# Optimization experiments

Hardware: AMD Instinct MI355X
Metric: run time of the kernel (lower is better)

Reference implementation:

```python
import jax, jax.numpy as jnp
import numpy as np

VOCAB, HIDDEN, LAYERS = 128, 1024, 2
B, T = 128, 512


def setup_inputs() -> dict:
    key = jax.random.key(0)
    ks = jax.random.split(key, 8)
    s0 = 1.0 / np.sqrt(HIDDEN)
    x = jax.random.normal(ks[0], (B, T, VOCAB), dtype=jnp.float32)
    h = jnp.zeros((LAYERS, B, HIDDEN), dtype=jnp.float32)
    c = jnp.zeros((LAYERS, B, HIDDEN), dtype=jnp.float32)
    # LSTM params, gate order (i, f, g, o) concatenated along last dim (4H)
    Wx0 = jax.random.uniform(ks[1], (VOCAB, 4 * HIDDEN), jnp.float32, -s0, s0)
    Wh0 = jax.random.uniform(ks[2], (HIDDEN, 4 * HIDDEN), jnp.float32, -s0, s0)
    b0 = jax.random.uniform(ks[3], (4 * HIDDEN,), jnp.float32, -s0, s0)
    Wx1 = jax.random.uniform(ks[4], (HIDDEN, 4 * HIDDEN), jnp.float32, -s0, s0)
    Wh1 = jax.random.uniform(ks[5], (HIDDEN, 4 * HIDDEN), jnp.float32, -s0, s0)
    b1 = jax.random.uniform(ks[6], (4 * HIDDEN,), jnp.float32, -s0, s0)
    return {"x": x, "h": h, "c": c, "Wx0": Wx0, "Wh0": Wh0, "b0": b0,
            "Wx1": Wx1, "Wh1": Wh1, "b1": b1}


def _lstm_cell(inp, h_prev, c_prev, Wx, Wh, b):
    gates = inp @ Wx + h_prev @ Wh + b            # (B, 4H)
    i, f, g, o = jnp.split(gates, 4, axis=-1)
    i = jax.nn.sigmoid(i)
    f = jax.nn.sigmoid(f)
    g = jnp.tanh(g)
    o = jax.nn.sigmoid(o)
    c_new = f * c_prev + i * g
    h_new = o * jnp.tanh(c_new)
    return h_new, c_new


def reference(x, h, c, Wx0, Wh0, b0, Wx1, Wh1, b1):
    layer_params = [(Wx0, Wh0, b0), (Wx1, Wh1, b1)]

    def step(carry, x_t):
        h_prev, c_prev = carry                    # each (L, B, H)
        inp = x_t                                 # (B, VOCAB)
        hs, cs = [], []
        for l, (Wx, Wh, b) in enumerate(layer_params):
            h_new, c_new = _lstm_cell(inp, h_prev[l], c_prev[l], Wx, Wh, b)
            hs.append(h_new)
            cs.append(c_new)
            inp = h_new
        return (jnp.stack(hs), jnp.stack(cs)), hs[-1]

    xs = jnp.swapaxes(x, 0, 1)                    # (T, B, VOCAB)
    (h_f, c_f), outs = jax.lax.scan(step, (h, c), xs)
    outs = jnp.swapaxes(outs, 0, 1)               # (B, T, H)
    return outs, h_f, c_f
```

## Files before the change

### kernel.cpp

```cpp
#include <hip/hip_runtime.h>

#define VV 128
#define HH 1024
#define BB 128
#define TT 512
#define G4 4096
#define BTH ((size_t)BB * TT * HH)
#define HPAR (4 * 64 * 512)
#define RING 32

typedef __attribute__((ext_vector_type(8))) short bf16x8;
typedef __attribute__((ext_vector_type(16))) float f32x16;

__device__ __forceinline__ short f2bf(float f) {
  unsigned u = __float_as_uint(f);
  u = (u + 0x7fffu + ((u >> 16) & 1u)) >> 16;
  return (short)u;
}

__device__ __forceinline__ float fsig(float x) {
  x = fminf(fmaxf(x, -30.f), 30.f);
  float e = __expf(-x);
  return 1.f / (1.f + e);
}
__device__ __forceinline__ float ftanh(float x) {
  x = fminf(fmaxf(x, -15.f), 15.f);
  float e = __expf(-2.f * x);
  return (1.f - e) / (1.f + e);
}

__device__ __forceinline__ unsigned eidx(int t) {
  return ((unsigned)(t + 1) * 37u) & (RING - 1);
}


__global__ void init_state(const float* __restrict__ h,
                           short* __restrict__ h0dst, short* __restrict__ h1dst) {
  const int n = 2 * HPAR;
  for (int i = blockIdx.x * blockDim.x + threadIdx.x; i < n; i += gridDim.x * blockDim.x) {
    int inner = i & (HPAR - 1);
    int l = i >> 17;
    int e = i & 7, lane = (i >> 3) & 63, kc = (i >> 9) & 63, rb = (i >> 15) & 3;
    int row = rb * 32 + (lane & 31);
    int j = kc * 16 + ((lane >> 5) << 3) + e;
    short hb = f2bf(h[((size_t)l * BB + row) * HH + j]);
    (l ? h1dst : h0dst)[inner] = hb;
  }
}

__global__ void pack_w(const float* __restrict__ Wx0, const float* __restrict__ Wh0,
                       const float* __restrict__ Wx1, const float* __restrict__ Wh1,
                       short* __restrict__ wp0, short* __restrict__ wp1) {
  const int n0 = 128 * 72 * 512;
  const int n1 = 128 * 128 * 512;
  for (int i = blockIdx.x * blockDim.x + threadIdx.x; i < n0 + n1; i += gridDim.x * blockDim.x) {
    if (i < n0) {
      int cu = i / (72 * 512);
      int rem = i - cu * (72 * 512);
      int kc = rem >> 9, le = rem & 511;
      int lane = le >> 3, e = le & 7;
      int k = kc * 16 + ((lane >> 5) << 3) + e;
      int cl = lane & 31;
      int gcol = (cl >> 3) * HH + cu * 8 + (cl & 7);
      float f = (k < VV) ? Wx0[(size_t)k * G4 + gcol] : Wh0[(size_t)(k - VV) * G4 + gcol];
      wp0[i] = f2bf(f);
    } else {
      int j = i - n0;
      int cu = j >> 16;
      int rem = j & 65535;
      int kc = rem >> 9, le = rem & 511;
      int lane = le >> 3, e = le & 7;
      int k = kc * 16 + ((lane >> 5) << 3) + e;
      int cl = lane & 31;
      int gcol = (cl >> 3) * HH + cu * 8 + (cl & 7);
      float f = (k < HH) ? Wx1[(size_t)k * G4 + gcol] : Wh1[(size_t)(k - HH) * G4 + gcol];
      wp1[j] = f2bf(f);
    }
  }
}

__global__ void pack_b(const float* __restrict__ b0, const float* __restrict__ b1,
                       float* __restrict__ bp, unsigned* __restrict__ slots) {
  int i = blockIdx.x * blockDim.x + threadIdx.x;
  if (i < 2 * 128 * 32) {
    int l = i >> 12;
    int cu = (i >> 5) & 127;
    int cc = i & 31;
    const float* b = l ? b1 : b0;
    bp[i] = b[(cc >> 3) * HH + cu * 8 + (cc & 7)];
  }
  if (i < 512) slots[i] = 0u;
}


template <int NCH, bool COH>
__device__ __forceinline__ void hgemm(f32x16* acc, const short* pa0, const short* pa1,
                                      const short* __restrict__ pb) {
  constexpr int NG = NCH / 16;
  bf16x8 A[3][16];
#pragma unroll
  for (int g = 0; g < 3; ++g) {
#pragma unroll
    for (int j = 0; j < 16; ++j) {
      const int c = g * 16 + j;
      const short* ap = (c < 64) ? (pa0 + c * 512) : (pa1 + (c - 64) * 512);
      if constexpr (COH)
        asm volatile("global_load_dwordx4 %0, %1, off sc0 sc1" : "=v"(A[g][j]) : "v"(ap));
      else
        asm volatile("global_load_dwordx4 %0, %1, off" : "=v"(A[g][j]) : "v"(ap));
    }
  }
#pragma unroll
  for (int g = 0; g < NG; ++g) {
    const int rem = NG - 1 - g;
    if (rem >= 2)      asm volatile("s_waitcnt vmcnt(32)" ::: "memory");
    else if (rem == 1) asm volatile("s_waitcnt vmcnt(16)" ::: "memory");
    else               asm volatile("s_waitcnt vmcnt(0)" ::: "memory");
#pragma unroll
    for (int j = 0; j < 16; ++j)
      asm volatile("" : "+v"(A[g % 3][j]));
#pragma unroll
    for (int j = 0; j < 16; ++j) {
      const int c = g * 16 + j;
      bf16x8 b = *(const bf16x8*)(pb + c * 512);
      acc[j & 3] = __builtin_amdgcn_mfma_f32_32x32x16_bf16(A[g % 3][j], b, acc[j & 3], 0, 0, 0);
    }
    if (g + 3 < NG) {
#pragma unroll
      for (int j = 0; j < 16; ++j) {
        const int c = (g + 3) * 16 + j;
        const short* ap = (c < 64) ? (pa0 + c * 512) : (pa1 + (c - 64) * 512);
        if constexpr (COH)
          asm volatile("global_load_dwordx4 %0, %1, off sc0 sc1"
                       : "=v"(A[(g + 3) % 3][j]) : "v"(ap));
        else
          asm volatile("global_load_dwordx4 %0, %1, off"
                       : "=v"(A[(g + 3) % 3][j]) : "v"(ap));
      }
    }
  }
}

__device__ __forceinline__ void xgemm_raw(f32x16* acc, const float* __restrict__ xlane,
                                          const short* __restrict__ pb) {
#pragma unroll
  for (int c = 0; c < 8; ++c) {
    float4 lo = *(const float4*)(xlane + c * 16);
    float4 hi = *(const float4*)(xlane + c * 16 + 4);
    bf16x8 a;
    a[0] = f2bf(lo.x); a[1] = f2bf(lo.y); a[2] = f2bf(lo.z); a[3] = f2bf(lo.w);
    a[4] = f2bf(hi.x); a[5] = f2bf(hi.y); a[6] = f2bf(hi.z); a[7] = f2bf(hi.w);
    bf16x8 b = *(const bf16x8*)(pb + c * 512);
    acc[c & 3] = __builtin_amdgcn_mfma_f32_32x32x16_bf16(a, b, acc[c & 3], 0, 0, 0);
  }
}

template <bool RINGM>
__global__ void __launch_bounds__(256, 1) lstm_main(const float* __restrict__ x,
    short* __restrict__ h0b, short* __restrict__ h1b,
    const short* __restrict__ wp0, const short* __restrict__ wp1,
    const float* __restrict__ bpack, const float* __restrict__ cin,
    float* __restrict__ out, unsigned* __restrict__ slots) {
  __shared__ short wlds[128 * 512];
  unsigned* gdone = slots + 256;
  const int blk = blockIdx.x;
  const int layer = blk >> 7;
  const int cu = blk & 127;
  const int tid = threadIdx.x;
  const int lane = tid & 63;
  const int wave = tid >> 6;

  const int nkc = layer ? 128 : 72;
  const short* wsrc = layer ? (wp1 + (size_t)cu * 128 * 512) : (wp0 + (size_t)cu * 72 * 512);
  for (int i = tid; i < nkc * 64; i += 256)
    ((int4*)wlds)[i] = ((const int4*)wsrc)[i];
  __syncthreads();

  const int col = lane & 31;
  const float bias = bpack[layer * 4096 + cu * 32 + col];
  const int uu = col & 7;
  const bool ewlane = (col < 8);
  const int gcol = cu * 8 + uu;
  const int hi4 = ((lane >> 5) << 2);
  const int arow = wave * 32 + col;
  const int koff = (lane >> 5) << 3;
  const float* xlane0 = x + (size_t)arow * (TT * VV) + koff;

  float creg[16], hval[16];
#pragma unroll
  for (int r = 0; r < 16; ++r) {
    int grow = wave * 32 + (r & 3) + ((r >> 2) << 3) + hi4;
    creg[r] = ewlane ? cin[(size_t)layer * BB * HH + (size_t)grow * HH + gcol] : 0.f;
    hval[r] = 0.f;
  }

  const int pst = (wave * 64 + (cu >> 1)) * 512 + ((cu & 1) << 8);
  const int wv64 = wave * 64 * 512 + lane * 8;

  f32x16 acc[4];
  auto initacc = [&]() {
#pragma unroll
    for (int r = 0; r < 16; ++r) {
      acc[0][r] = bias; acc[1][r] = 0.f; acc[2][r] = 0.f; acc[3][r] = 0.f;
    }
  };

  if (layer == 0) {
    initacc();
    xgemm_raw(acc, xlane0, wlds + lane * 8);
  }

  for (int p = 0; p <= TT; ++p) {
    if (p > 0) {
      const unsigned tgt = (unsigned)p;
      if ((blk & 31) == 0 && tid < 32) {
        for (;;) {
          unsigned v = __hip_atomic_load(&slots[blk + tid],
                                         __ATOMIC_RELAXED, __HIP_MEMORY_SCOPE_AGENT);
          if (__all(v >= tgt)) break;
          __builtin_amdgcn_s_sleep(1);
        }
        if (tid == 0)
          __hip_atomic_store(&gdone[(blk >> 5) << 5], tgt,
                             __ATOMIC_RELAXED, __HIP_MEMORY_SCOPE_AGENT);
      }
      if (tid < 8) {
        for (;;) {
          unsigned v = __hip_atomic_load(&gdone[tid << 5],
                                         __ATOMIC_RELAXED, __HIP_MEMORY_SCOPE_AGENT);
          if (__all(v >= tgt)) break;
          __builtin_amdgcn_s_sleep(1);
        }
      }
      __syncthreads();
    }

    const bool active = layer ? (p >= 1) : (p < TT);
    const int t = layer ? (p - 1) : p;
    if (active) {
      const short *ra0, *ra1;
      if constexpr (RINGM) {
        ra0 = h0b + (size_t)eidx(p - 1) * HPAR + wv64;
        ra1 = h1b + (size_t)eidx(p - 2) * HPAR + wv64;
      } else {
        ra0 = h0b + (size_t)((p + 1) & 1) * HPAR + wv64;
        ra1 = h1b + (size_t)(p & 1) * HPAR + wv64;
      }
      if (layer == 0) {
        hgemm<64, !RINGM>(acc, ra0, ra0, wlds + 8 * 512 + lane * 8);
      } else {
        initacc();
        hgemm<128, !RINGM>(acc, ra0, ra1, wlds + lane * 8);
      }
      f32x16 accf = (acc[0] + acc[1]) + (acc[2] + acc[3]);
      short* hp;
      if constexpr (RINGM)
        hp = layer ? (h1b + (size_t)eidx(p - 1) * HPAR)
                   : (h0b + (size_t)eidx(p) * HPAR);
      else
        hp = layer ? (h1b + (size_t)((p + 1) & 1) * HPAR)
                   : (h0b + (size_t)(p & 1) * HPAR);
#pragma unroll
      for (int r = 0; r < 16; ++r) {
        float a0 = accf[r];
        float nl = (col >= 16 && col < 24) ? ftanh(a0) : fsig(a0);
        float f_ = __shfl_xor(nl, 8);
        float g_ = __shfl_xor(nl, 16);
        float o_ = __shfl_xor(nl, 24);
        const int rloc = (r & 3) + ((r >> 2) << 3) + hi4;
        const int grow = wave * 32 + rloc;
        float hnew = 0.f;
        if (ewlane) {
          float cnew = f_ * creg[r] + nl * g_;
          creg[r] = cnew;
          hnew = o_ * ftanh(cnew);
          hval[r] = hnew;
        }
        unsigned hb = (unsigned short)f2bf(hnew);
        unsigned pb2 = (unsigned)__shfl_xor((int)hb, 1);
        if (ewlane) {
          if (t == TT - 1) {
            out[BTH + (size_t)layer * BB * HH + (size_t)grow * HH + gcol] = hnew;
            out[BTH + (size_t)(2 + layer) * BB * HH + (size_t)grow * HH + gcol] = creg[r];
          }
          if (!(uu & 1)) {
            unsigned dw = hb | (pb2 << 16);
            __hip_atomic_store((unsigned*)(hp + pst + rloc * 8 + uu), dw,
                               __ATOMIC_RELAXED, __HIP_MEMORY_SCOPE_AGENT);
          }
        }
      }
    }

    if (p == TT) {
      if (layer && active && ewlane) {
#pragma unroll
        for (int r = 0; r < 16; ++r) {
          const int rloc = (r & 3) + ((r >> 2) << 3) + hi4;
          const int grow = wave * 32 + rloc;
          out[(size_t)grow * TT * HH + (size_t)t * HH + gcol] = hval[r];
        }
      }
      break;
    }

    __syncthreads();
    if (tid == 0)
      __hip_atomic_store(&slots[blk], (unsigned)(p + 1),
                         __ATOMIC_RELAXED, __HIP_MEMORY_SCOPE_AGENT);

    if (layer == 0) {
      if (p + 1 < TT) {
        initacc();
        xgemm_raw(acc, xlane0 + (size_t)(p + 1) * VV, wlds + lane * 8);
      }
    } else if (active && ewlane) {
#pragma unroll
      for (int r = 0; r < 16; ++r) {
        const int rloc = (r & 3) + ((r >> 2) << 3) + hi4;
        const int grow = wave * 32 + rloc;
        out[(size_t)grow * TT * HH + (size_t)t * HH + gcol] = hval[r];
      }
    }
  }
}


extern "C" void kernel_launch(void* const* d_in, const int* in_sizes, int n_in,
                              void* d_out, int out_size, void* d_ws, size_t ws_size,
                              hipStream_t stream) {
  const float* x   = (const float*)d_in[0];
  const float* h   = (const float*)d_in[1];
  const float* c   = (const float*)d_in[2];
  const float* Wx0 = (const float*)d_in[3];
  const float* Wh0 = (const float*)d_in[4];
  const float* b0  = (const float*)d_in[5];
  const float* Wx1 = (const float*)d_in[6];
  const float* Wh1 = (const float*)d_in[7];
  const float* b1  = (const float*)d_in[8];
  float* out = (float*)d_out;

  char* ws = (char*)d_ws;
  short* wp0 = (short*)ws;
  short* wp1 = (short*)(ws + 9437184);
  float* bp  = (float*)(ws + 26214400);
  unsigned* slots = (unsigned*)(ws + 26247168);
  short* h0r = (short*)(ws + 26249216);
  short* h1r = (short*)(ws + 34637824);
  const size_t need_ring = 43026432;
  short* h0p = h0r;
  short* h1p = (short*)(ws + 26249216 + 1048576);

  const bool ring = (ws_size >= need_ring);
  short* h0ini = ring ? h0r : (h0p + HPAR);
  short* h1ini = ring ? h1r : (h1p + HPAR);

  hipLaunchKernelGGL(init_state, dim3(512),  dim3(256), 0, stream, h, h0ini, h1ini);
  hipLaunchKernelGGL(pack_w,     dim3(4096), dim3(256), 0, stream, Wx0, Wh0, Wx1, Wh1, wp0, wp1);
  hipLaunchKernelGGL(pack_b,     dim3(32),   dim3(256), 0, stream, b0, b1, bp, slots);

  if (ring)
    hipLaunchKernelGGL((lstm_main<true>), dim3(256), dim3(256), 0, stream,
                       x, h0r, h1r, wp0, wp1, bp, c, out, slots);
  else
    hipLaunchKernelGGL((lstm_main<false>), dim3(256), dim3(256), 0, stream,
                       x, h0p, h1p, wp0, wp1, bp, c, out, slots);
}
```

Measured before the change: 6.485 ms.

## Stage h in LDS for vector stores, concentrate relays, drop ping-pong path

```diff
diff --git a/kernel.cpp b/kernel.cpp
--- a/kernel.cpp
+++ b/kernel.cpp
@@ -93,7 +93,7 @@
 }
 
 
-template <int NCH, bool COH>
+template <int NCH>
 __device__ __forceinline__ void hgemm(f32x16* acc, const short* pa0, const short* pa1,
                                       const short* __restrict__ pb) {
   constexpr int NG = NCH / 16;
@@ -104,10 +104,7 @@
     for (int j = 0; j < 16; ++j) {
       const int c = g * 16 + j;
       const short* ap = (c < 64) ? (pa0 + c * 512) : (pa1 + (c - 64) * 512);
-      if constexpr (COH)
-        asm volatile("global_load_dwordx4 %0, %1, off sc0 sc1" : "=v"(A[g][j]) : "v"(ap));
-      else
-        asm volatile("global_load_dwordx4 %0, %1, off" : "=v"(A[g][j]) : "v"(ap));
+      asm volatile("global_load_dwordx4 %0, %1, off" : "=v"(A[g][j]) : "v"(ap));
     }
   }
 #pragma unroll
@@ -130,12 +127,8 @@
       for (int j = 0; j < 16; ++j) {
         const int c = (g + 3) * 16 + j;
         const short* ap = (c < 64) ? (pa0 + c * 512) : (pa1 + (c - 64) * 512);
-        if constexpr (COH)
-          asm volatile("global_load_dwordx4 %0, %1, off sc0 sc1"
-                       : "=v"(A[(g + 3) % 3][j]) : "v"(ap));
-        else
-          asm volatile("global_load_dwordx4 %0, %1, off"
-                       : "=v"(A[(g + 3) % 3][j]) : "v"(ap));
+        asm volatile("global_load_dwordx4 %0, %1, off"
+                     : "=v"(A[(g + 3) % 3][j]) : "v"(ap));
       }
     }
   }
@@ -155,13 +148,13 @@
   }
 }
 
-template <bool RINGM>
 __global__ void __launch_bounds__(256, 1) lstm_main(const float* __restrict__ x,
     short* __restrict__ h0b, short* __restrict__ h1b,
     const short* __restrict__ wp0, const short* __restrict__ wp1,
     const float* __restrict__ bpack, const float* __restrict__ cin,
     float* __restrict__ out, unsigned* __restrict__ slots) {
   __shared__ short wlds[128 * 512];
+  __shared__ short hstage[4][256];
   unsigned* gdone = slots + 256;
   const int blk = blockIdx.x;
   const int layer = blk >> 7;
@@ -169,6 +162,8 @@
   const int tid = threadIdx.x;
   const int lane = tid & 63;
   const int wave = tid >> 6;
+  const bool isRelay = ((blk & 15) == 0) && (blk < 128);
+  const int rbase = (blk >> 4) << 5;
 
   const int nkc = layer ? 128 : 72;
   const short* wsrc = layer ? (wp1 + (size_t)cu * 128 * 512) : (wp0 + (size_t)cu * 72 * 512);
@@ -213,15 +208,14 @@
   for (int p = 0; p <= TT; ++p) {
     if (p > 0) {
       const unsigned tgt = (unsigned)p;
-      if ((blk & 31) == 0 && tid < 32) {
+      if (isRelay && tid < 32) {
         for (;;) {
-          unsigned v = __hip_atomic_load(&slots[blk + tid],
+          unsigned v = __hip_atomic_load(&slots[rbase + tid],
                                          __ATOMIC_RELAXED, __HIP_MEMORY_SCOPE_AGENT);
           if (__all(v >= tgt)) break;
-          __builtin_amdgcn_s_sleep(1);
         }
         if (tid == 0)
-          __hip_atomic_store(&gdone[(blk >> 5) << 5], tgt,
+          __hip_atomic_store(&gdone[(blk >> 4) << 5], tgt,
                              __ATOMIC_RELAXED, __HIP_MEMORY_SCOPE_AGENT);
       }
       if (tid < 8) {
@@ -238,28 +232,15 @@
     const bool active = layer ? (p >= 1) : (p < TT);
     const int t = layer ? (p - 1) : p;
     if (active) {
-      const short *ra0, *ra1;
-      if constexpr (RINGM) {
-        ra0 = h0b + (size_t)eidx(p - 1) * HPAR + wv64;
-        ra1 = h1b + (size_t)eidx(p - 2) * HPAR + wv64;
-      } else {
-        ra0 = h0b + (size_t)((p + 1) & 1) * HPAR + wv64;
-        ra1 = h1b + (size_t)(p & 1) * HPAR + wv64;
-      }
+      const short* ra0 = h0b + (size_t)eidx(p - 1) * HPAR + wv64;
+      const short* ra1 = h1b + (size_t)eidx(p - 2) * HPAR + wv64;
       if (layer == 0) {
-        hgemm<64, !RINGM>(acc, ra0, ra0, wlds + 8 * 512 + lane * 8);
+        hgemm<64>(acc, ra0, ra0, wlds + 8 * 512 + lane * 8);
       } else {
         initacc();
-        hgemm<128, !RINGM>(acc, ra0, ra1, wlds + lane * 8);
+        hgemm<128>(acc, ra0, ra1, wlds + lane * 8);
       }
       f32x16 accf = (acc[0] + acc[1]) + (acc[2] + acc[3]);
-      short* hp;
-      if constexpr (RINGM)
-        hp = layer ? (h1b + (size_t)eidx(p - 1) * HPAR)
-                   : (h0b + (size_t)eidx(p) * HPAR);
-      else
-        hp = layer ? (h1b + (size_t)((p + 1) & 1) * HPAR)
-                   : (h0b + (size_t)(p & 1) * HPAR);
 #pragma unroll
       for (int r = 0; r < 16; ++r) {
         float a0 = accf[r];
@@ -275,20 +256,22 @@
           creg[r] = cnew;
           hnew = o_ * ftanh(cnew);
           hval[r] = hnew;
-        }
-        unsigned hb = (unsigned short)f2bf(hnew);
-        unsigned pb2 = (unsigned)__shfl_xor((int)hb, 1);
-        if (ewlane) {
+          hstage[wave][rloc * 8 + uu] = f2bf(hnew);
           if (t == TT - 1) {
             out[BTH + (size_t)layer * BB * HH + (size_t)grow * HH + gcol] = hnew;
             out[BTH + (size_t)(2 + layer) * BB * HH + (size_t)grow * HH + gcol] = creg[r];
           }
-          if (!(uu & 1)) {
-            unsigned dw = hb | (pb2 << 16);
-            __hip_atomic_store((unsigned*)(hp + pst + rloc * 8 + uu), dw,
-                               __ATOMIC_RELAXED, __HIP_MEMORY_SCOPE_AGENT);
-          }
-        }
+        }
+      }
+      if (p < TT) {
+        short* hp = (layer ? h1b + (size_t)eidx(p - 1) * HPAR
+                           : h0b + (size_t)eidx(p) * HPAR) + pst;
+        if (lane < 32) {
+          bf16x8 v = *(const bf16x8*)&hstage[wave][lane * 8];
+          asm volatile("global_store_dwordx4 %0, %1, off sc0 sc1"
+                       :: "v"(hp + lane * 8), "v"(v) : "memory");
+        }
+        asm volatile("s_waitcnt vmcnt(0)" ::: "memory");
       }
     }
 
@@ -347,22 +330,11 @@
   unsigned* slots = (unsigned*)(ws + 26247168);
   short* h0r = (short*)(ws + 26249216);
   short* h1r = (short*)(ws + 34637824);
-  const size_t need_ring = 43026432;
-  short* h0p = h0r;
-  short* h1p = (short*)(ws + 26249216 + 1048576);
-
-  const bool ring = (ws_size >= need_ring);
-  short* h0ini = ring ? h0r : (h0p + HPAR);
-  short* h1ini = ring ? h1r : (h1p + HPAR);
-
-  hipLaunchKernelGGL(init_state, dim3(512),  dim3(256), 0, stream, h, h0ini, h1ini);
+
+  hipLaunchKernelGGL(init_state, dim3(512),  dim3(256), 0, stream, h, h0r, h1r);
   hipLaunchKernelGGL(pack_w,     dim3(4096), dim3(256), 0, stream, Wx0, Wh0, Wx1, Wh1, wp0, wp1);
   hipLaunchKernelGGL(pack_b,     dim3(32),   dim3(256), 0, stream, b0, b1, bp, slots);
 
-  if (ring)
-    hipLaunchKernelGGL((lstm_main<true>), dim3(256), dim3(256), 0, stream,
-                       x, h0r, h1r, wp0, wp1, bp, c, out, slots);
-  else
-    hipLaunchKernelGGL((lstm_main<false>), dim3(256), dim3(256), 0, stream,
-                       x, h0p, h1p, wp0, wp1, bp, c, out, slots);
-}
+  hipLaunchKernelGGL(lstm_main, dim3(256), dim3(256), 0, stream,
+                     x, h0r, h1r, wp0, wp1, bp, c, out, slots);
+}
```

Result: no change. 6.391 ms (-1.4%).
